# Performance work log

Measured on AMD Instinct MI355X. Metric: run time of the kernel, lower is better.

Reference implementation:

```python
import jax, jax.numpy as jnp
import numpy as np


def setup_inputs() -> dict:
    key = jax.random.key(0)
    k1, k2 = jax.random.split(key)
    B, N, LENGTH = 2048, 64, 8
    # x: (batch, 2, n, n) -- real/imag planes of batched complex matrices
    x = jax.random.normal(k1, (B, 2, N, N), dtype=jnp.float32) * 0.1
    # learned coefficients: (length, 2, n, n), scaled down like the factorial-decaying init
    coefficients = jax.random.normal(k2, (LENGTH, 2, N, N), dtype=jnp.float32) * 0.05
    return {"x": x, "coefficients": coefficients}


def reference(x, coefficients):
    # Faithful port of MatrixMPowerSeriesLayer.call (including the sign used
    # for res_imag inside the i>=2 loop, which differs from the i==1 term).
    length = coefficients.shape[0]
    n = x.shape[2]
    xr = x[:, 0]  # (b, n, n)
    xi = x[:, 1]
    cr = coefficients[:, 0]  # (length, n, n)
    ci = coefficients[:, 1]
    unit = jnp.eye(n, dtype=x.dtype)

    tr, ti = xr, xi  # running complex power x^p
    # order-0 term: unit @ c[0] (broadcasts against batched terms)
    res_r = unit @ cr[0] + (jnp.einsum('bjk,kl->bjl', tr, cr[1]) - jnp.einsum('bjk,kl->bjl', ti, ci[1]))
    res_i = unit @ ci[0] + (jnp.einsum('bjk,kl->bjl', tr, ci[1]) + jnp.einsum('bjk,kl->bjl', ti, cr[1]))

    for i in range(2, length):
        # complex batched matmul: tmp <- tmp @ x
        new_tr = jnp.einsum('bjk,bkl->bjl', tr, xr) - jnp.einsum('bjk,bkl->bjl', ti, xi)
        ti = jnp.einsum('bjk,bkl->bjl', tr, xi) + jnp.einsum('bjk,bkl->bjl', ti, xr)
        tr = new_tr
        res_r = res_r + jnp.einsum('bjk,kl->bjl', tr, cr[i]) - jnp.einsum('bjk,kl->bjl', ti, ci[i])
        # NOTE: original code subtracts ti @ cr[i] here (not adds) -- kept faithful.
        res_i = res_i + jnp.einsum('bjk,kl->bjl', tr, ci[i]) - jnp.einsum('bjk,kl->bjl', ti, cr[i])

    return jnp.stack([res_r, res_i], axis=1)  # (b, 2, n, n)
```

## Files before the change

### kernel.cpp

```cpp
#include <hip/hip_runtime.h>

typedef __attribute__((ext_vector_type(4))) short short4v;
typedef __attribute__((ext_vector_type(8))) short short8v;
typedef __attribute__((ext_vector_type(4))) unsigned int uint4v;
typedef __attribute__((ext_vector_type(4))) float f32x4;
typedef __attribute__((ext_vector_type(16))) float f32x16;

#define LSTRIDE 68
#define MATB (64 * LSTRIDE * 2)
#define REGA 0
#define REGB (4 * MATB)
#define LDS_BYTES (8 * MATB)

#define CFRAG_BYTES (7 * 4 * 2 * 4 * 1024)
#define INIT_OFF CFRAG_BYTES

__device__ __forceinline__ short bf16h(float v) {
    union { float f; unsigned u; } x; x.f = v;
    unsigned r = x.u + 0x7FFFu + ((x.u >> 16) & 1u);
    return (short)(r >> 16);
}
__device__ __forceinline__ float bf16tof(short s) {
    union { unsigned u; float f; } x; x.u = ((unsigned)(unsigned short)s) << 16;
    return x.f;
}
__device__ __forceinline__ f32x16 MF(short8v a, short8v b, f32x16 c) {
    return __builtin_amdgcn_mfma_f32_32x32x16_bf16(a, b, c, 0, 0, 0);
}
__device__ __forceinline__ short8v negf(short8v a) {
    uint4v u = __builtin_bit_cast(uint4v, a);
    u ^= 0x80008000u;
    return __builtin_bit_cast(short8v, u);
}

__global__ void pms_prep(const float* __restrict__ coef, char* __restrict__ wsb) {
    const int blk = blockIdx.x;
    const int lane = threadIdx.x;
    const int lrow = lane & 31, lhi = lane >> 5;
    if (blk < 56) {
        const int qr  = blk & 1;
        const int km  = blk >> 1;
        const int mat = km & 3;
        const int kk  = km >> 2;
        const int part = mat >> 1;
        const int lo   = mat & 1;
        const float* C = coef + (size_t)((kk + 1) * 2 + part) * 4096;
        for (int t = 0; t < 4; ++t) {
            short8v o;
            #pragma unroll
            for (int j = 0; j < 8; ++j) {
                int krow = 16 * t + 8 * lhi + j;
                int col  = 32 * qr + lrow;
                float v = C[krow * 64 + col];
                short hh = bf16h(v);
                o[j] = lo ? bf16h(v - bf16tof(hh)) : hh;
            }
            *(short8v*)(wsb + ((size_t)blk * 4 + t) * 1024 + lane * 16) = o;
        }
    } else {
        const int id = blk - 56;
        const int qc = id & 1, qr = (id >> 1) & 1, part = id >> 2;
        const float* C0 = coef + (size_t)part * 4096;
        float* dst = (float*)(wsb + INIT_OFF + (size_t)(((part * 2 + qr) * 2 + qc) * 64 + lane) * 64);
        #pragma unroll
        for (int v = 0; v < 16; ++v) {
            int r = 32 * qr + (v & 3) + 8 * (v >> 2) + 4 * lhi;
            int c = 32 * qc + lrow;
            dst[v] = C0[c * 64 + r];
        }
    }
}

__global__ __launch_bounds__(256, 2) void pms_main(
    const float* __restrict__ x, const char* __restrict__ wsb,
    float* __restrict__ out)
{
    extern __shared__ char smem[];
    const int tid  = threadIdx.x;
    const int lane = tid & 63;
    const int w    = tid >> 6;
    const int qr = w >> 1, qc = w & 1;
    const int lrow = lane & 31, lhi = lane >> 5;
    const size_t b = blockIdx.x;
    const float* xb = x + b * 8192;

    #pragma unroll
    for (int s = 0; s < 8; ++s) {
        int f = s * 1024 + tid * 4;
        int p = f >> 12, m = (f >> 6) & 63, c = f & 63;
        f32x4 v = *(const f32x4*)(xb + f);
        short4v h, l;
        #pragma unroll
        for (int j = 0; j < 4; ++j) {
            short hh = bf16h(v[j]);
            h[j] = hh;
            l[j] = bf16h(v[j] - bf16tof(hh));
        }
        int off = (m * LSTRIDE + c) * 2;
        *(short4v*)(smem + REGA + (p * 2 + 0) * MATB + off) = h;
        *(short4v*)(smem + REGA + (p * 2 + 1) * MATB + off) = l;
    }
    __syncthreads();

    short8v xa[2][2][4];
    #pragma unroll
    for (int pi = 0; pi < 2; ++pi)
    #pragma unroll
    for (int hl = 0; hl < 2; ++hl)
    #pragma unroll
    for (int t = 0; t < 4; ++t) {
        const short* mp = (const short*)(smem + REGA + (pi * 2 + hl) * MATB);
        short8v a;
        #pragma unroll
        for (int j = 0; j < 8; ++j)
            a[j] = mp[(16 * t + 8 * lhi + j) * LSTRIDE + 32 * qr + lrow];
        xa[pi][hl][t] = a;
    }

    f32x16 accRr, accRi;
    {
        const f32x4* p0 = (const f32x4*)(wsb + INIT_OFF + (size_t)(((0 + qr) * 2 + qc) * 64 + lane) * 64);
        const f32x4* p1 = (const f32x4*)(wsb + INIT_OFF + (size_t)(((2 + qr) * 2 + qc) * 64 + lane) * 64);
        #pragma unroll
        for (int g = 0; g < 4; ++g) {
            f32x4 a = p0[g], c4 = p1[g];
            #pragma unroll
            for (int j = 0; j < 4; ++j) { accRr[4 * g + j] = a[j]; accRi[4 * g + j] = c4[j]; }
        }
    }

    auto ldB = [&](int rbase, int mat, int t) -> short8v {
        const short4v* p = (const short4v*)(smem + rbase + mat * MATB
                             + (32 * qc + lrow) * (LSTRIDE * 2) + 32 * t + 16 * lhi);
        short4v a = p[0], c4 = p[1];
        short8v r;
        #pragma unroll
        for (int j = 0; j < 4; ++j) { r[j] = a[j]; r[j + 4] = c4[j]; }
        return r;
    };

    int cur = REGA, nxt = REGB;

    for (int k = 2; k <= 7; ++k) {
        const char* cw = wsb + (size_t)(k - 2) * 32768;
        const bool k1 = (k == 2);
        f32x16 aTr, aTi;
        #pragma unroll
        for (int v = 0; v < 16; ++v) { aTr[v] = 0.f; aTi[v] = 0.f; }

        #pragma unroll
        for (int t = 0; t < 4; ++t) {
            short8v cRh = *(const short8v*)(cw + ((0 * 2 + qr) * 4 + t) * 1024 + lane * 16);
            short8v cRl = *(const short8v*)(cw + ((1 * 2 + qr) * 4 + t) * 1024 + lane * 16);
            short8v cIh = *(const short8v*)(cw + ((2 * 2 + qr) * 4 + t) * 1024 + lane * 16);
            short8v cIl = *(const short8v*)(cw + ((3 * 2 + qr) * 4 + t) * 1024 + lane * 16);
            short8v Brh = ldB(cur, 0, t), Brl = ldB(cur, 1, t);
            short8v Bih = ldB(cur, 2, t), Bil = ldB(cur, 3, t);
            short8v nBih = negf(Bih), nBil = negf(Bil);
            short8v sBih = k1 ? Bih : nBih;
            short8v sBil = k1 ? Bil : nBil;

            accRr = MF(cRh, Brh, accRr);
            accRi = MF(cIh, Brh, accRi);
            aTr   = MF(xa[0][0][t], Brh, aTr);
            aTi   = MF(xa[1][0][t], Brh, aTi);

            accRr = MF(cRh, Brl, accRr);
            accRi = MF(cIh, Brl, accRi);
            aTr   = MF(xa[0][0][t], Brl, aTr);
            aTi   = MF(xa[1][0][t], Brl, aTi);

            accRr = MF(cRl, Brh, accRr);
            accRi = MF(cIl, Brh, accRi);
            aTr   = MF(xa[0][1][t], Brh, aTr);
            aTi   = MF(xa[1][1][t], Brh, aTi);

            accRr = MF(cIh, nBih, accRr);
            accRi = MF(cRh, sBih, accRi);
            aTr   = MF(xa[1][0][t], nBih, aTr);
            aTi   = MF(xa[0][0][t], Bih, aTi);

            accRr = MF(cIh, nBil, accRr);
            accRi = MF(cRh, sBil, accRi);
            aTr   = MF(xa[1][0][t], nBil, aTr);
            aTi   = MF(xa[0][0][t], Bil, aTi);

            accRr = MF(cIl, nBih, accRr);
            accRi = MF(cRl, sBih, accRi);
            aTr   = MF(xa[1][1][t], nBih, aTr);
            aTi   = MF(xa[0][1][t], Bih, aTi);
        }

        {
            const int c = 32 * qc + lrow;
            #pragma unroll
            for (int g = 0; g < 4; ++g) {
                int rbse = 32 * qr + 8 * g + 4 * lhi;
                short4v hr, lr4, hi4, li4;
                #pragma unroll
                for (int j = 0; j < 4; ++j) {
                    float vr = aTr[4 * g + j];
                    short hh = bf16h(vr);
                    hr[j] = hh; lr4[j] = bf16h(vr - bf16tof(hh));
                    float vi = aTi[4 * g + j];
                    short h2 = bf16h(vi);
                    hi4[j] = h2; li4[j] = bf16h(vi - bf16tof(h2));
                }
                int off = (c * LSTRIDE + rbse) * 2;
                *(short4v*)(smem + nxt + 0 * MATB + off) = hr;
                *(short4v*)(smem + nxt + 1 * MATB + off) = lr4;
                *(short4v*)(smem + nxt + 2 * MATB + off) = hi4;
                *(short4v*)(smem + nxt + 3 * MATB + off) = li4;
            }
        }
        __syncthreads();
        int tmp = cur; cur = nxt; nxt = tmp;
    }

    {
        const char* cw = wsb + (size_t)6 * 32768;
        #pragma unroll
        for (int t = 0; t < 4; ++t) {
            short8v cRh = *(const short8v*)(cw + ((0 * 2 + qr) * 4 + t) * 1024 + lane * 16);
            short8v cRl = *(const short8v*)(cw + ((1 * 2 + qr) * 4 + t) * 1024 + lane * 16);
            short8v cIh = *(const short8v*)(cw + ((2 * 2 + qr) * 4 + t) * 1024 + lane * 16);
            short8v cIl = *(const short8v*)(cw + ((3 * 2 + qr) * 4 + t) * 1024 + lane * 16);
            short8v Brh = ldB(cur, 0, t), Brl = ldB(cur, 1, t);
            short8v Bih = ldB(cur, 2, t), Bil = ldB(cur, 3, t);
            short8v nBih = negf(Bih), nBil = negf(Bil);

            accRr = MF(cRh, Brh, accRr);
            accRi = MF(cIh, Brh, accRi);
            accRr = MF(cRh, Brl, accRr);
            accRi = MF(cIh, Brl, accRi);
            accRr = MF(cRl, Brh, accRr);
            accRi = MF(cIl, Brh, accRi);
            accRr = MF(cIh, nBih, accRr);
            accRi = MF(cRh, nBih, accRi);
            accRr = MF(cIh, nBil, accRr);
            accRi = MF(cRh, nBil, accRi);
            accRr = MF(cIl, nBih, accRr);
            accRi = MF(cRl, nBih, accRi);
        }
    }

    {
        const int c = 32 * qc + lrow;
        #pragma unroll
        for (int g = 0; g < 4; ++g) {
            int rbse = 32 * qr + 8 * g + 4 * lhi;
            f32x4 vr, vi;
            #pragma unroll
            for (int j = 0; j < 4; ++j) { vr[j] = accRr[4 * g + j]; vi[j] = accRi[4 * g + j]; }
            *(f32x4*)(smem + nxt + (size_t)(0 * 4352 + c * LSTRIDE + rbse) * 4) = vr;
            *(f32x4*)(smem + nxt + (size_t)(1 * 4352 + c * LSTRIDE + rbse) * 4) = vi;
        }
    }
    __syncthreads();
    float* ob = out + b * 8192;
    #pragma unroll
    for (int s = 0; s < 8; ++s) {
        int f = s * 1024 + tid * 4;
        int p = f >> 12, m = (f >> 6) & 63, n = f & 63;
        *(f32x4*)(ob + f) = *(const f32x4*)(smem + nxt + (size_t)(p * 4352 + m * LSTRIDE + n) * 4);
    }
}

extern "C" void kernel_launch(void* const* d_in, const int* in_sizes, int n_in,
                              void* d_out, int out_size, void* d_ws, size_t ws_size,
                              hipStream_t stream) {
    const float* x    = (const float*)d_in[0];
    const float* coef = (const float*)d_in[1];
    float* out = (float*)d_out;
    char*  wsb = (char*)d_ws;
    const int B = in_sizes[0] / 8192;

    (void)hipFuncSetAttribute(reinterpret_cast<const void*>(&pms_main),
                              hipFuncAttributeMaxDynamicSharedMemorySize, LDS_BYTES);

    pms_prep<<<64, 64, 0, stream>>>(coef, wsb);
    pms_main<<<B, 256, LDS_BYTES, stream>>>(x, wsb, out);
}
```

Before: 164.1 us.

## Single-buffer LDS power matrix and use packed bf16 conversion for hi/lo split

Drops the ping-pong LDS buffers for the running power matrix and uses one buffer, with an extra barrier before each overwrite. This halves LDS per block (about 70KB to 35KB), so launch bounds rise to 3 blocks per CU to improve occupancy. The hi/lo bf16 split now uses the packed v_cvt_pk_bf16_f32 instruction, replacing manual rounding, to cut VALU work. The cost is an added __syncthreads per iteration. Register limits under 3 blocks per CU may also cause spills.

Result: faster. 157.8 us (-3.9%).

```diff
diff --git a/kernel.cpp b/kernel.cpp
--- a/kernel.cpp
+++ b/kernel.cpp
@@ -2,15 +2,14 @@
 
 typedef __attribute__((ext_vector_type(4))) short short4v;
 typedef __attribute__((ext_vector_type(8))) short short8v;
+typedef __attribute__((ext_vector_type(2))) unsigned int uint2v;
 typedef __attribute__((ext_vector_type(4))) unsigned int uint4v;
 typedef __attribute__((ext_vector_type(4))) float f32x4;
 typedef __attribute__((ext_vector_type(16))) float f32x16;
 
 #define LSTRIDE 68
 #define MATB (64 * LSTRIDE * 2)
-#define REGA 0
-#define REGB (4 * MATB)
-#define LDS_BYTES (8 * MATB)
+#define LDS_BYTES (4 * MATB)
 
 #define CFRAG_BYTES (7 * 4 * 2 * 4 * 1024)
 #define INIT_OFF CFRAG_BYTES
@@ -23,6 +22,17 @@
 __device__ __forceinline__ float bf16tof(short s) {
     union { unsigned u; float f; } x; x.u = ((unsigned)(unsigned short)s) << 16;
     return x.f;
+}
+struct HL { unsigned h, l; };
+__device__ __forceinline__ HL split2(float v0, float v1) {
+    unsigned hp, lp;
+    asm("v_cvt_pk_bf16_f32 %0, %1, %2" : "=v"(hp) : "v"(v0), "v"(v1));
+    union { unsigned u; float f; } a, b;
+    a.u = hp << 16;
+    b.u = hp & 0xffff0000u;
+    float l0 = v0 - a.f, l1 = v1 - b.f;
+    asm("v_cvt_pk_bf16_f32 %0, %1, %2" : "=v"(lp) : "v"(l0), "v"(l1));
+    HL r; r.h = hp; r.l = lp; return r;
 }
 __device__ __forceinline__ f32x16 MF(short8v a, short8v b, f32x16 c) {
     return __builtin_amdgcn_mfma_f32_32x32x16_bf16(a, b, c, 0, 0, 0);
@@ -71,7 +81,7 @@
     }
 }
 
-__global__ __launch_bounds__(256, 2) void pms_main(
+__global__ __launch_bounds__(256, 3) void pms_main(
     const float* __restrict__ x, const char* __restrict__ wsb,
     float* __restrict__ out)
 {
@@ -89,16 +99,14 @@
         int f = s * 1024 + tid * 4;
         int p = f >> 12, m = (f >> 6) & 63, c = f & 63;
         f32x4 v = *(const f32x4*)(xb + f);
-        short4v h, l;
-        #pragma unroll
-        for (int j = 0; j < 4; ++j) {
-            short hh = bf16h(v[j]);
-            h[j] = hh;
-            l[j] = bf16h(v[j] - bf16tof(hh));
-        }
+        HL a01 = split2(v[0], v[1]);
+        HL a23 = split2(v[2], v[3]);
+        uint2v h, l;
+        h[0] = a01.h; l[0] = a01.l;
+        h[1] = a23.h; l[1] = a23.l;
         int off = (m * LSTRIDE + c) * 2;
-        *(short4v*)(smem + REGA + (p * 2 + 0) * MATB + off) = h;
-        *(short4v*)(smem + REGA + (p * 2 + 1) * MATB + off) = l;
+        *(uint2v*)(smem + (p * 2 + 0) * MATB + off) = h;
+        *(uint2v*)(smem + (p * 2 + 1) * MATB + off) = l;
     }
     __syncthreads();
 
@@ -109,7 +117,7 @@
     for (int hl = 0; hl < 2; ++hl)
     #pragma unroll
     for (int t = 0; t < 4; ++t) {
-        const short* mp = (const short*)(smem + REGA + (pi * 2 + hl) * MATB);
+        const short* mp = (const short*)(smem + (pi * 2 + hl) * MATB);
         short8v a;
         #pragma unroll
         for (int j = 0; j < 8; ++j)
@@ -129,8 +137,8 @@
         }
     }
 
-    auto ldB = [&](int rbase, int mat, int t) -> short8v {
-        const short4v* p = (const short4v*)(smem + rbase + mat * MATB
+    auto ldB = [&](int mat, int t) -> short8v {
+        const short4v* p = (const short4v*)(smem + mat * MATB
                              + (32 * qc + lrow) * (LSTRIDE * 2) + 32 * t + 16 * lhi);
         short4v a = p[0], c4 = p[1];
         short8v r;
@@ -138,8 +146,6 @@
         for (int j = 0; j < 4; ++j) { r[j] = a[j]; r[j + 4] = c4[j]; }
         return r;
     };
-
-    int cur = REGA, nxt = REGB;
 
     for (int k = 2; k <= 7; ++k) {
         const char* cw = wsb + (size_t)(k - 2) * 32768;
@@ -154,8 +160,8 @@
             short8v cRl = *(const short8v*)(cw + ((1 * 2 + qr) * 4 + t) * 1024 + lane * 16);
             short8v cIh = *(const short8v*)(cw + ((2 * 2 + qr) * 4 + t) * 1024 + lane * 16);
             short8v cIl = *(const short8v*)(cw + ((3 * 2 + qr) * 4 + t) * 1024 + lane * 16);
-            short8v Brh = ldB(cur, 0, t), Brl = ldB(cur, 1, t);
-            short8v Bih = ldB(cur, 2, t), Bil = ldB(cur, 3, t);
+            short8v Brh = ldB(0, t), Brl = ldB(1, t);
+            short8v Bih = ldB(2, t), Bil = ldB(3, t);
             short8v nBih = negf(Bih), nBil = negf(Bil);
             short8v sBih = k1 ? Bih : nBih;
             short8v sBil = k1 ? Bil : nBil;
@@ -191,30 +197,28 @@
             aTi   = MF(xa[0][1][t], Bih, aTi);
         }
 
+        __syncthreads();
+
         {
             const int c = 32 * qc + lrow;
             #pragma unroll
             for (int g = 0; g < 4; ++g) {
                 int rbse = 32 * qr + 8 * g + 4 * lhi;
-                short4v hr, lr4, hi4, li4;
-                #pragma unroll
-                for (int j = 0; j < 4; ++j) {
-                    float vr = aTr[4 * g + j];
-                    short hh = bf16h(vr);
-                    hr[j] = hh; lr4[j] = bf16h(vr - bf16tof(hh));
-                    float vi = aTi[4 * g + j];
-                    short h2 = bf16h(vi);
-                    hi4[j] = h2; li4[j] = bf16h(vi - bf16tof(h2));
-                }
+                HL r01 = split2(aTr[4 * g + 0], aTr[4 * g + 1]);
+                HL r23 = split2(aTr[4 * g + 2], aTr[4 * g + 3]);
+                HL i01 = split2(aTi[4 * g + 0], aTi[4 * g + 1]);
+                HL i23 = split2(aTi[4 * g + 2], aTi[4 * g + 3]);
+                uint2v hr, lr, hi2, li2;
+                hr[0] = r01.h; lr[0] = r01.l; hr[1] = r23.h; lr[1] = r23.l;
+                hi2[0] = i01.h; li2[0] = i01.l; hi2[1] = i23.h; li2[1] = i23.l;
                 int off = (c * LSTRIDE + rbse) * 2;
-                *(short4v*)(smem + nxt + 0 * MATB + off) = hr;
-                *(short4v*)(smem + nxt + 1 * MATB + off) = lr4;
-                *(short4v*)(smem + nxt + 2 * MATB + off) = hi4;
-                *(short4v*)(smem + nxt + 3 * MATB + off) = li4;
+                *(uint2v*)(smem + 0 * MATB + off) = hr;
+                *(uint2v*)(smem + 1 * MATB + off) = lr;
+                *(uint2v*)(smem + 2 * MATB + off) = hi2;
+                *(uint2v*)(smem + 3 * MATB + off) = li2;
             }
         }
         __syncthreads();
-        int tmp = cur; cur = nxt; nxt = tmp;
     }
 
     {
@@ -225,8 +229,8 @@
             short8v cRl = *(const short8v*)(cw + ((1 * 2 + qr) * 4 + t) * 1024 + lane * 16);
             short8v cIh = *(const short8v*)(cw + ((2 * 2 + qr) * 4 + t) * 1024 + lane * 16);
             short8v cIl = *(const short8v*)(cw + ((3 * 2 + qr) * 4 + t) * 1024 + lane * 16);
-            short8v Brh = ldB(cur, 0, t), Brl = ldB(cur, 1, t);
-            short8v Bih = ldB(cur, 2, t), Bil = ldB(cur, 3, t);
+            short8v Brh = ldB(0, t), Brl = ldB(1, t);
+            short8v Bih = ldB(2, t), Bil = ldB(3, t);
             short8v nBih = negf(Bih), nBil = negf(Bil);
 
             accRr = MF(cRh, Brh, accRr);
@@ -244,6 +248,7 @@
         }
     }
 
+    __syncthreads();
     {
         const int c = 32 * qc + lrow;
         #pragma unroll
@@ -252,8 +257,8 @@
             f32x4 vr, vi;
             #pragma unroll
             for (int j = 0; j < 4; ++j) { vr[j] = accRr[4 * g + j]; vi[j] = accRi[4 * g + j]; }
-            *(f32x4*)(smem + nxt + (size_t)(0 * 4352 + c * LSTRIDE + rbse) * 4) = vr;
-            *(f32x4*)(smem + nxt + (size_t)(1 * 4352 + c * LSTRIDE + rbse) * 4) = vi;
+            *(f32x4*)(smem + (size_t)(0 * 4352 + c * LSTRIDE + rbse) * 4) = vr;
+            *(f32x4*)(smem + (size_t)(1 * 4352 + c * LSTRIDE + rbse) * 4) = vi;
         }
     }
     __syncthreads();
@@ -262,7 +267,7 @@
     for (int s = 0; s < 8; ++s) {
         int f = s * 1024 + tid * 4;
         int p = f >> 12, m = (f >> 6) & 63, n = f & 63;
-        *(f32x4*)(ob + f) = *(const f32x4*)(smem + nxt + (size_t)(p * 4352 + m * LSTRIDE + n) * 4);
+        *(f32x4*)(ob + f) = *(const f32x4*)(smem + (size_t)(p * 4352 + m * LSTRIDE + n) * 4);
     }
 }
 
@@ -275,9 +280,6 @@
     char*  wsb = (char*)d_ws;
     const int B = in_sizes[0] / 8192;
 
-    (void)hipFuncSetAttribute(reinterpret_cast<const void*>(&pms_main),
-                              hipFuncAttributeMaxDynamicSharedMemorySize, LDS_BYTES);
-
     pms_prep<<<64, 64, 0, stream>>>(coef, wsb);
     pms_main<<<B, 256, LDS_BYTES, stream>>>(x, wsb, out);
 }
```
